# Kernel optimization log

Measured on AMD Instinct MI355X. Metric: run time of the kernel, lower is better.

## Reference

```python
import jax, jax.numpy as jnp
import numpy as np

D_MODEL = 512
H = 8


def setup_inputs() -> dict:
    key = jax.random.key(0)
    ks = jax.random.split(key, 11)
    B, L, D = 8, 1024, D_MODEL
    s = 1.0 / np.sqrt(D)
    return {
        "q": jax.random.normal(ks[0], (B, L, D), jnp.float32),
        "k": jax.random.normal(ks[1], (B, L, D), jnp.float32),
        "v": jax.random.normal(ks[2], (B, L, D), jnp.float32),
        "Wq": jax.random.normal(ks[3], (D, D), jnp.float32) * s,
        "bq": jnp.zeros((D,), jnp.float32),
        "Wk": jax.random.normal(ks[4], (D, D), jnp.float32) * s,
        "bk": jnp.zeros((D,), jnp.float32),
        "Wv": jax.random.normal(ks[5], (D, D), jnp.float32) * s,
        "bv": jnp.zeros((D,), jnp.float32),
        "Wo": jax.random.normal(ks[6], (D, D), jnp.float32) * s,
        "bo": jnp.zeros((D,), jnp.float32),
    }


def _split_heads(x, h):
    B, L, D = x.shape
    return x.reshape(B, L, h, D // h).transpose(0, 2, 1, 3)  # (B,h,L,dk)


def reference(q, k, v, Wq, bq, Wk, bk, Wv, bv, Wo, bo):
    B, L, D = q.shape
    dk = D // H
    qw = q @ Wq + bq
    kw = k @ Wk + bk
    vw = q @ Wv + bv  # faithful to source bug: dense_v applied to q, not v
    qh = _split_heads(qw, H)
    kh = _split_heads(kw, H)
    vh = _split_heads(vw, H)
    scale = jnp.asarray(1.0 / np.sqrt(dk), qh.dtype)
    scores = jnp.einsum("bhqd,bhkd->bhqk", qh, kh) * scale  # (B,h,L,L)
    attn = jax.nn.softmax(scores, axis=-1)
    ctx = jnp.einsum("bhqk,bhkd->bhqd", attn, vh)  # (B,h,L,dk)
    out = ctx.transpose(0, 2, 1, 3).reshape(B, L, D) @ Wo + bo
    return out, attn
```

## Files before the change

kernel.cpp:

```cpp
#include <hip/hip_runtime.h>

typedef unsigned short u16;
typedef __bf16 bf16x8 __attribute__((ext_vector_type(8)));
typedef unsigned short u16x8 __attribute__((ext_vector_type(8)));
typedef unsigned short u16x4 __attribute__((ext_vector_type(4)));
typedef float f32x4 __attribute__((ext_vector_type(4)));

#define MFMA16(a, b, c) __builtin_amdgcn_mfma_f32_16x16x32_bf16(a, b, c, 0, 0, 0)

__device__ __forceinline__ u16 f2bf(float f) {
    union { float f; unsigned u; } v; v.f = f;
    unsigned r = v.u + 0x7fffu + ((v.u >> 16) & 1u);
    return (u16)(r >> 16);
}

__global__ __launch_bounds__(256) void wtrans(const float* Wq, const float* Wk,
                                              const float* Wv, const float* Wo, u16* WT) {
    __shared__ float t[32][33];
    const int z = blockIdx.z;
    const float* W = (z == 0) ? Wq : (z == 1) ? Wk : (z == 2) ? Wv : Wo;
    u16* out = WT + (size_t)z * 512 * 512;
    const int tx = threadIdx.x;
    const int ty = threadIdx.y;
    const int k0 = blockIdx.y * 32;
    const int n0 = blockIdx.x * 32;
#pragma unroll
    for (int p = 0; p < 4; ++p)
        t[ty + 8 * p][tx] = W[(size_t)(k0 + ty + 8 * p) * 512 + n0 + tx];
    __syncthreads();
#pragma unroll
    for (int p = 0; p < 4; ++p) {
        const int n = n0 + ty + 8 * p;
        out[(size_t)n * 512 + k0 + tx] = f2bf(t[tx][ty + 8 * p]);
    }
}

template <bool A_F32, bool C_F32>
__device__ __forceinline__ void gemm_core(const void* Ap, const u16* Bt,
                                          const float* bias, void* Cp,
                                          int bm, int bn) {
    __shared__ u16 As[128 * 72];
    __shared__ u16 Bs[128 * 72];
    const int tid  = threadIdx.x;
    const int lane = tid & 63;
    const int w    = tid >> 6;
    const int wm   = (w >> 1) * 64;
    const int wn   = (w & 1) * 64;
    const int col  = lane & 15;
    const int quad = lane >> 4;

    f32x4 acc[4][4] = {};

    for (int kt = 0; kt < 512; kt += 64) {
        __syncthreads();
        if (A_F32) {
            const float* Af = (const float*)Ap;
            const int kg = (tid & 15) * 4;
            const int r0 = tid >> 4;
#pragma unroll
            for (int p = 0; p < 8; ++p) {
                const int r = r0 + p * 16;
                const float4 vv = *(const float4*)(Af + (size_t)(bm * 128 + r) * 512 + kt + kg);
                u16x4 o4;
                o4[0] = f2bf(vv.x); o4[1] = f2bf(vv.y); o4[2] = f2bf(vv.z); o4[3] = f2bf(vv.w);
                *(u16x4*)(As + r * 72 + kg) = o4;
            }
        } else {
            const u16* Ab = (const u16*)Ap;
            const int kg = (tid & 7) * 8;
            const int r0 = tid >> 3;
#pragma unroll
            for (int p = 0; p < 4; ++p) {
                const int r = r0 + p * 32;
                const u16x8 vv = *(const u16x8*)(Ab + (size_t)(bm * 128 + r) * 512 + kt + kg);
                *(u16x8*)(As + r * 72 + kg) = vv;
            }
        }
        {
            const int kg = (tid & 7) * 8;
            const int r0 = tid >> 3;
#pragma unroll
            for (int p = 0; p < 4; ++p) {
                const int n = r0 + p * 32;
                const u16x8 vv = *(const u16x8*)(Bt + (size_t)(bn * 128 + n) * 512 + kt + kg);
                *(u16x8*)(Bs + n * 72 + kg) = vv;
            }
        }
        __syncthreads();
#pragma unroll
        for (int ks = 0; ks < 2; ++ks) {
            const int k0 = ks * 32 + quad * 8;
            bf16x8 af[4], bfr[4];
#pragma unroll
            for (int i = 0; i < 4; ++i)
                af[i] = __builtin_bit_cast(bf16x8, *(const u16x8*)(As + (wm + i * 16 + col) * 72 + k0));
#pragma unroll
            for (int j = 0; j < 4; ++j)
                bfr[j] = __builtin_bit_cast(bf16x8, *(const u16x8*)(Bs + (wn + j * 16 + col) * 72 + k0));
#pragma unroll
            for (int i = 0; i < 4; ++i)
#pragma unroll
                for (int j = 0; j < 4; ++j)
                    acc[i][j] = MFMA16(af[i], bfr[j], acc[i][j]);
        }
    }
#pragma unroll
    for (int j = 0; j < 4; ++j) {
        const int gn = bn * 128 + wn + j * 16 + col;
        const float bv = bias[gn];
#pragma unroll
        for (int i = 0; i < 4; ++i) {
#pragma unroll
            for (int r = 0; r < 4; ++r) {
                const int gm = bm * 128 + wm + i * 16 + quad * 4 + r;
                const float val = acc[i][j][r] + bv;
                if (C_F32) ((float*)Cp)[(size_t)gm * 512 + gn] = val;
                else       ((u16*)Cp)[(size_t)gm * 512 + gn]   = f2bf(val);
            }
        }
    }
}

__global__ __launch_bounds__(256) void qkv_gemm(const float* q, const float* k, const u16* WT,
                                                const float* bq, const float* bk, const float* bv,
                                                u16* out) {
    const int z = blockIdx.z;
    const float* A    = (z == 1) ? k : q;
    const u16* B      = WT + (size_t)z * 512 * 512;
    const float* bias = (z == 0) ? bq : (z == 1) ? bk : bv;
    u16* C            = out + (size_t)z * 8192 * 512;
    gemm_core<true, false>(A, B, bias, C, blockIdx.x, blockIdx.y);
}

__global__ __launch_bounds__(256) void out_gemm(const u16* ctx, const u16* WoT,
                                                const float* bo, float* out) {
    gemm_core<false, true>(ctx, WoT, bo, out, blockIdx.x, blockIdx.y);
}

__global__ __launch_bounds__(256) void attn_kernel(const u16* qw, const u16* kw, const u16* vw,
                                                   float* attn_out, u16* ctx) {
    __shared__ u16 Qs[128 * 72];
    __shared__ u16 Ks[64 * 72];
    __shared__ u16 Vt[64 * 72];
    __shared__ u16 Ps[4][32 * 72];

    const int qt  = blockIdx.x;
    const int bh  = blockIdx.y;
    const int b   = bh >> 3, h = bh & 7;
    const int tid = threadIdx.x;
    const int lane = tid & 63, w = tid >> 6;
    const int col = lane & 15, quad = lane >> 4;
    const int wq  = w * 32;
    const float scale = 0.125f;

    const size_t headbase = (size_t)b * 1024 * 512 + (size_t)h * 64;

    {
        const int kg = (tid & 7) * 8;
        const int r0 = tid >> 3;
#pragma unroll
        for (int p = 0; p < 4; ++p) {
            const int r = r0 + p * 32;
            const u16x8 vv = *(const u16x8*)(qw + headbase + (size_t)(qt * 128 + r) * 512 + kg);
            *(u16x8*)(Qs + r * 72 + kg) = vv;
        }
    }

    float m_i[2][4], l_i[2][4];
#pragma unroll
    for (int i = 0; i < 2; ++i)
#pragma unroll
        for (int r = 0; r < 4; ++r) { m_i[i][r] = -1e30f; l_i[i][r] = 0.f; }

    for (int kt = 0; kt < 16; ++kt) {
        __syncthreads();
        {
            const int kg = (tid & 7) * 8;
            const int r0 = tid >> 3;
#pragma unroll
            for (int p = 0; p < 2; ++p) {
                const int key = r0 + p * 32;
                const u16x8 vv = *(const u16x8*)(kw + headbase + (size_t)(kt * 64 + key) * 512 + kg);
                *(u16x8*)(Ks + key * 72 + kg) = vv;
            }
        }
        __syncthreads();
        f32x4 s[2][4] = {};
#pragma unroll
        for (int ks = 0; ks < 2; ++ks) {
            const int k0 = ks * 32 + quad * 8;
            bf16x8 qf[2], kf[4];
#pragma unroll
            for (int i = 0; i < 2; ++i)
                qf[i] = __builtin_bit_cast(bf16x8, *(const u16x8*)(Qs + (wq + i * 16 + col) * 72 + k0));
#pragma unroll
            for (int j = 0; j < 4; ++j)
                kf[j] = __builtin_bit_cast(bf16x8, *(const u16x8*)(Ks + (j * 16 + col) * 72 + k0));
#pragma unroll
            for (int i = 0; i < 2; ++i)
#pragma unroll
                for (int j = 0; j < 4; ++j)
                    s[i][j] = MFMA16(qf[i], kf[j], s[i][j]);
        }
#pragma unroll
        for (int i = 0; i < 2; ++i) {
#pragma unroll
            for (int r = 0; r < 4; ++r) {
                float tm = fmaxf(fmaxf(s[i][0][r], s[i][1][r]), fmaxf(s[i][2][r], s[i][3][r])) * scale;
                tm = fmaxf(tm, __shfl_xor(tm, 1));
                tm = fmaxf(tm, __shfl_xor(tm, 2));
                tm = fmaxf(tm, __shfl_xor(tm, 4));
                tm = fmaxf(tm, __shfl_xor(tm, 8));
                const float mn = fmaxf(m_i[i][r], tm);
                float ps = 0.f;
#pragma unroll
                for (int j = 0; j < 4; ++j) ps += __expf(s[i][j][r] * scale - mn);
                ps += __shfl_xor(ps, 1);
                ps += __shfl_xor(ps, 2);
                ps += __shfl_xor(ps, 4);
                ps += __shfl_xor(ps, 8);
                const float alpha = __expf(m_i[i][r] - mn);
                l_i[i][r] = l_i[i][r] * alpha + ps;
                m_i[i][r] = mn;
            }
        }
    }

    float rinv[2][4];
#pragma unroll
    for (int i = 0; i < 2; ++i)
#pragma unroll
        for (int r = 0; r < 4; ++r) rinv[i][r] = 1.0f / l_i[i][r];

    f32x4 o[2][4] = {};

    for (int kt = 0; kt < 16; ++kt) {
        __syncthreads();
        {
            const int kg = (tid & 7) * 8;
            const int r0 = tid >> 3;
#pragma unroll
            for (int p = 0; p < 2; ++p) {
                const int key = r0 + p * 32;
                const u16x8 vv = *(const u16x8*)(kw + headbase + (size_t)(kt * 64 + key) * 512 + kg);
                *(u16x8*)(Ks + key * 72 + kg) = vv;
            }
        }
        {
            const int key = tid & 63;
            const int ob  = tid >> 6;
#pragma unroll
            for (int p = 0; p < 2; ++p) {
                const int oct = ob + 4 * p;
                const u16x8 vv = *(const u16x8*)(vw + headbase + (size_t)(kt * 64 + key) * 512 + oct * 8);
#pragma unroll
                for (int e = 0; e < 8; ++e)
                    Vt[(oct * 8 + e) * 72 + key] = vv[e];
            }
        }
        __syncthreads();
        f32x4 s[2][4] = {};
#pragma unroll
        for (int ks = 0; ks < 2; ++ks) {
            const int k0 = ks * 32 + quad * 8;
            bf16x8 qf[2], kf[4];
#pragma unroll
            for (int i = 0; i < 2; ++i)
                qf[i] = __builtin_bit_cast(bf16x8, *(const u16x8*)(Qs + (wq + i * 16 + col) * 72 + k0));
#pragma unroll
            for (int j = 0; j < 4; ++j)
                kf[j] = __builtin_bit_cast(bf16x8, *(const u16x8*)(Ks + (j * 16 + col) * 72 + k0));
#pragma unroll
            for (int i = 0; i < 2; ++i)
#pragma unroll
                for (int j = 0; j < 4; ++j)
                    s[i][j] = MFMA16(qf[i], kf[j], s[i][j]);
        }
        const size_t abase = ((size_t)bh * 1024 + (size_t)(qt * 128)) * 1024 + (size_t)kt * 64;
#pragma unroll
        for (int i = 0; i < 2; ++i) {
#pragma unroll
            for (int j = 0; j < 4; ++j) {
                const int kk = j * 16 + col;
#pragma unroll
                for (int r = 0; r < 4; ++r) {
                    const int qm = wq + i * 16 + quad * 4 + r;
                    const float p = __expf(s[i][j][r] * scale - m_i[i][r]) * rinv[i][r];
                    attn_out[abase + (size_t)qm * 1024 + kk] = p;
                    Ps[w][(i * 16 + quad * 4 + r) * 72 + kk] = f2bf(p);
                }
            }
        }
        bf16x8 vfrag[2][4];
#pragma unroll
        for (int ks = 0; ks < 2; ++ks) {
            const int k0 = ks * 32 + quad * 8;
#pragma unroll
            for (int j = 0; j < 4; ++j)
                vfrag[ks][j] = __builtin_bit_cast(bf16x8, *(const u16x8*)(Vt + (j * 16 + col) * 72 + k0));
        }
#pragma unroll
        for (int i = 0; i < 2; ++i) {
#pragma unroll
            for (int ks = 0; ks < 2; ++ks) {
                const int k0 = ks * 32 + quad * 8;
                const bf16x8 pf = __builtin_bit_cast(bf16x8, *(const u16x8*)(&Ps[w][(i * 16 + col) * 72 + k0]));
#pragma unroll
                for (int j = 0; j < 4; ++j)
                    o[i][j] = MFMA16(pf, vfrag[ks][j], o[i][j]);
            }
        }
    }

#pragma unroll
    for (int i = 0; i < 2; ++i)
#pragma unroll
        for (int j = 0; j < 4; ++j)
#pragma unroll
            for (int r = 0; r < 4; ++r) {
                const int qg = qt * 128 + wq + i * 16 + quad * 4 + r;
                const int dk = j * 16 + col;
                ctx[(size_t)(b * 1024 + qg) * 512 + h * 64 + dk] = f2bf(o[i][j][r]);
            }
}

extern "C" void kernel_launch(void* const* d_in, const int* in_sizes, int n_in,
                              void* d_out, int out_size, void* d_ws, size_t ws_size,
                              hipStream_t stream) {
    (void)in_sizes; (void)n_in; (void)out_size; (void)ws_size;
    const float* q  = (const float*)d_in[0];
    const float* k  = (const float*)d_in[1];
    const float* Wq = (const float*)d_in[3];
    const float* bq = (const float*)d_in[4];
    const float* Wk = (const float*)d_in[5];
    const float* bk = (const float*)d_in[6];
    const float* Wv = (const float*)d_in[7];
    const float* bv = (const float*)d_in[8];
    const float* Wo = (const float*)d_in[9];
    const float* bo = (const float*)d_in[10];

    float* out  = (float*)d_out;
    float* attn = (float*)d_out + (size_t)8 * 1024 * 512;

    char* ws = (char*)d_ws;
    u16* WT  = (u16*)ws;
    u16* qkv = (u16*)(ws + (size_t)4 * 512 * 512 * 2);
    u16* qw  = qkv;
    u16* kw  = qkv + (size_t)8192 * 512;
    u16* vw  = qkv + (size_t)2 * 8192 * 512;
    u16* ctx = (u16*)(ws + (size_t)4 * 512 * 512 * 2 + (size_t)3 * 8192 * 512 * 2);

    wtrans   <<<dim3(16, 16, 4), dim3(32, 8), 0, stream>>>(Wq, Wk, Wv, Wo, WT);
    qkv_gemm <<<dim3(64, 4, 3),  256,          0, stream>>>(q, k, WT, bq, bk, bv, qkv);
    attn_kernel<<<dim3(8, 64),   256,          0, stream>>>(qw, kw, vw, attn, ctx);
    out_gemm <<<dim3(64, 4),     256,          0, stream>>>(ctx, WT + (size_t)3 * 512 * 512, bo, out);
}
```

Measured before the change: 451.5 us.

## Restructure attention to 8 waves, drop max tracking, vectorize attn stores, preconvert inputs

The attention kernel moves to 512 threads, with each wave owning 16 query rows and keeping its Q fragments in registers instead of shared memory. The first pass no longer tracks a running max and only sums unshifted exponentials. Probabilities are staged through shared memory so the attention matrix can be written with float4 stores. A separate kernel converts q and k to bf16 once, so the GEMM loads bf16 directly, and the GEMMs get occupancy hints. Skipping the max subtraction risks overflow for large scores, and the written attention values are now bf16-rounded.

```diff
diff --git a/kernel.cpp b/kernel.cpp
--- a/kernel.cpp
+++ b/kernel.cpp
@@ -12,6 +12,10 @@
     union { float f; unsigned u; } v; v.f = f;
     unsigned r = v.u + 0x7fffu + ((v.u >> 16) & 1u);
     return (u16)(r >> 16);
+}
+__device__ __forceinline__ float bf2f(u16 u) {
+    union { unsigned u; float f; } v; v.u = (unsigned)u << 16;
+    return v.f;
 }
 
 __global__ __launch_bounds__(256) void wtrans(const float* Wq, const float* Wk,
@@ -20,10 +24,8 @@
     const int z = blockIdx.z;
     const float* W = (z == 0) ? Wq : (z == 1) ? Wk : (z == 2) ? Wv : Wo;
     u16* out = WT + (size_t)z * 512 * 512;
-    const int tx = threadIdx.x;
-    const int ty = threadIdx.y;
-    const int k0 = blockIdx.y * 32;
-    const int n0 = blockIdx.x * 32;
+    const int tx = threadIdx.x, ty = threadIdx.y;
+    const int k0 = blockIdx.y * 32, n0 = blockIdx.x * 32;
 #pragma unroll
     for (int p = 0; p < 4; ++p)
         t[ty + 8 * p][tx] = W[(size_t)(k0 + ty + 8 * p) * 512 + n0 + tx];
@@ -35,8 +37,19 @@
     }
 }
 
-template <bool A_F32, bool C_F32>
-__device__ __forceinline__ void gemm_core(const void* Ap, const u16* Bt,
+__global__ __launch_bounds__(256) void qkconv(const float* q, const float* k, u16* qb, u16* kb) {
+    const size_t n4 = (size_t)8192 * 512 / 4;
+    const size_t stride = (size_t)gridDim.x * 256;
+    for (size_t i = (size_t)blockIdx.x * 256 + threadIdx.x; i < 2 * n4; i += stride) {
+        const float4 v = (i < n4) ? ((const float4*)q)[i] : ((const float4*)k)[i - n4];
+        u16x4 o;
+        o[0] = f2bf(v.x); o[1] = f2bf(v.y); o[2] = f2bf(v.z); o[3] = f2bf(v.w);
+        if (i < n4) ((u16x4*)qb)[i] = o; else ((u16x4*)kb)[i - n4] = o;
+    }
+}
+
+template <bool C_F32>
+__device__ __forceinline__ void gemm_core(const u16* A, const u16* Bt,
                                           const float* bias, void* Cp,
                                           int bm, int bn) {
     __shared__ u16 As[128 * 72];
@@ -53,37 +66,16 @@
 
     for (int kt = 0; kt < 512; kt += 64) {
         __syncthreads();
-        if (A_F32) {
-            const float* Af = (const float*)Ap;
-            const int kg = (tid & 15) * 4;
-            const int r0 = tid >> 4;
-#pragma unroll
-            for (int p = 0; p < 8; ++p) {
-                const int r = r0 + p * 16;
-                const float4 vv = *(const float4*)(Af + (size_t)(bm * 128 + r) * 512 + kt + kg);
-                u16x4 o4;
-                o4[0] = f2bf(vv.x); o4[1] = f2bf(vv.y); o4[2] = f2bf(vv.z); o4[3] = f2bf(vv.w);
-                *(u16x4*)(As + r * 72 + kg) = o4;
-            }
-        } else {
-            const u16* Ab = (const u16*)Ap;
+        {
             const int kg = (tid & 7) * 8;
             const int r0 = tid >> 3;
 #pragma unroll
             for (int p = 0; p < 4; ++p) {
                 const int r = r0 + p * 32;
-                const u16x8 vv = *(const u16x8*)(Ab + (size_t)(bm * 128 + r) * 512 + kt + kg);
-                *(u16x8*)(As + r * 72 + kg) = vv;
-            }
-        }
-        {
-            const int kg = (tid & 7) * 8;
-            const int r0 = tid >> 3;
-#pragma unroll
-            for (int p = 0; p < 4; ++p) {
-                const int n = r0 + p * 32;
-                const u16x8 vv = *(const u16x8*)(Bt + (size_t)(bn * 128 + n) * 512 + kt + kg);
-                *(u16x8*)(Bs + n * 72 + kg) = vv;
+                *(u16x8*)(As + r * 72 + kg) =
+                    *(const u16x8*)(A + (size_t)(bm * 128 + r) * 512 + kt + kg);
+                *(u16x8*)(Bs + r * 72 + kg) =
+                    *(const u16x8*)(Bt + (size_t)(bn * 128 + r) * 512 + kt + kg);
             }
         }
         __syncthreads();
@@ -121,28 +113,27 @@
     }
 }
 
-__global__ __launch_bounds__(256) void qkv_gemm(const float* q, const float* k, const u16* WT,
-                                                const float* bq, const float* bk, const float* bv,
-                                                u16* out) {
+__global__ __launch_bounds__(256, 3) void qkv_gemm(const u16* qb, const u16* kb, const u16* WT,
+                                                   const float* bq, const float* bk, const float* bv,
+                                                   u16* out) {
     const int z = blockIdx.z;
-    const float* A    = (z == 1) ? k : q;
+    const u16* A      = (z == 1) ? kb : qb;
     const u16* B      = WT + (size_t)z * 512 * 512;
     const float* bias = (z == 0) ? bq : (z == 1) ? bk : bv;
     u16* C            = out + (size_t)z * 8192 * 512;
-    gemm_core<true, false>(A, B, bias, C, blockIdx.x, blockIdx.y);
-}
-
-__global__ __launch_bounds__(256) void out_gemm(const u16* ctx, const u16* WoT,
-                                                const float* bo, float* out) {
-    gemm_core<false, true>(ctx, WoT, bo, out, blockIdx.x, blockIdx.y);
-}
-
-__global__ __launch_bounds__(256) void attn_kernel(const u16* qw, const u16* kw, const u16* vw,
-                                                   float* attn_out, u16* ctx) {
-    __shared__ u16 Qs[128 * 72];
+    gemm_core<false>(A, B, bias, C, blockIdx.x, blockIdx.y);
+}
+
+__global__ __launch_bounds__(256, 3) void out_gemm(const u16* ctx, const u16* WoT,
+                                                   const float* bo, float* out) {
+    gemm_core<true>(ctx, WoT, bo, out, blockIdx.x, blockIdx.y);
+}
+
+__global__ __launch_bounds__(512, 4) void attn_kernel(const u16* qw, const u16* kw, const u16* vw,
+                                                      float* attn_out, u16* ctx) {
     __shared__ u16 Ks[64 * 72];
     __shared__ u16 Vt[64 * 72];
-    __shared__ u16 Ps[4][32 * 72];
+    __shared__ u16 Ps[8][16 * 72];
 
     const int qt  = blockIdx.x;
     const int bh  = blockIdx.y;
@@ -150,178 +141,120 @@
     const int tid = threadIdx.x;
     const int lane = tid & 63, w = tid >> 6;
     const int col = lane & 15, quad = lane >> 4;
-    const int wq  = w * 32;
+    const int wq  = w * 16;
     const float scale = 0.125f;
 
     const size_t headbase = (size_t)b * 1024 * 512 + (size_t)h * 64;
 
+    bf16x8 qf[2];
     {
-        const int kg = (tid & 7) * 8;
-        const int r0 = tid >> 3;
-#pragma unroll
-        for (int p = 0; p < 4; ++p) {
-            const int r = r0 + p * 32;
-            const u16x8 vv = *(const u16x8*)(qw + headbase + (size_t)(qt * 128 + r) * 512 + kg);
-            *(u16x8*)(Qs + r * 72 + kg) = vv;
-        }
-    }
-
-    float m_i[2][4], l_i[2][4];
-#pragma unroll
-    for (int i = 0; i < 2; ++i)
-#pragma unroll
-        for (int r = 0; r < 4; ++r) { m_i[i][r] = -1e30f; l_i[i][r] = 0.f; }
+        const size_t qrow = headbase + (size_t)(qt * 128 + wq + col) * 512 + quad * 8;
+        qf[0] = __builtin_bit_cast(bf16x8, *(const u16x8*)(qw + qrow));
+        qf[1] = __builtin_bit_cast(bf16x8, *(const u16x8*)(qw + qrow + 32));
+    }
+
+    float l_acc[4] = {0.f, 0.f, 0.f, 0.f};
 
     for (int kt = 0; kt < 16; ++kt) {
         __syncthreads();
         {
-            const int kg = (tid & 7) * 8;
-            const int r0 = tid >> 3;
-#pragma unroll
-            for (int p = 0; p < 2; ++p) {
-                const int key = r0 + p * 32;
-                const u16x8 vv = *(const u16x8*)(kw + headbase + (size_t)(kt * 64 + key) * 512 + kg);
-                *(u16x8*)(Ks + key * 72 + kg) = vv;
-            }
-        }
-        __syncthreads();
-        f32x4 s[2][4] = {};
-#pragma unroll
-        for (int ks = 0; ks < 2; ++ks) {
-            const int k0 = ks * 32 + quad * 8;
-            bf16x8 qf[2], kf[4];
-#pragma unroll
-            for (int i = 0; i < 2; ++i)
-                qf[i] = __builtin_bit_cast(bf16x8, *(const u16x8*)(Qs + (wq + i * 16 + col) * 72 + k0));
+            const int key = tid >> 3, kg = (tid & 7) * 8;
+            *(u16x8*)(Ks + key * 72 + kg) =
+                *(const u16x8*)(kw + headbase + (size_t)(kt * 64 + key) * 512 + kg);
+        }
+        __syncthreads();
+        f32x4 s[4] = {};
+#pragma unroll
+        for (int ks = 0; ks < 2; ++ks) {
+            const int k0 = ks * 32 + quad * 8;
+            bf16x8 kf[4];
 #pragma unroll
             for (int j = 0; j < 4; ++j)
                 kf[j] = __builtin_bit_cast(bf16x8, *(const u16x8*)(Ks + (j * 16 + col) * 72 + k0));
 #pragma unroll
-            for (int i = 0; i < 2; ++i)
-#pragma unroll
-                for (int j = 0; j < 4; ++j)
-                    s[i][j] = MFMA16(qf[i], kf[j], s[i][j]);
-        }
-#pragma unroll
-        for (int i = 0; i < 2; ++i) {
+            for (int j = 0; j < 4; ++j)
+                s[j] = MFMA16(qf[ks], kf[j], s[j]);
+        }
+#pragma unroll
+        for (int r = 0; r < 4; ++r)
+            l_acc[r] += __expf(s[0][r] * scale) + __expf(s[1][r] * scale) +
+                        __expf(s[2][r] * scale) + __expf(s[3][r] * scale);
+    }
+
+    float rinv[4];
+#pragma unroll
+    for (int r = 0; r < 4; ++r) {
+        float l = l_acc[r];
+        l += __shfl_xor(l, 1); l += __shfl_xor(l, 2);
+        l += __shfl_xor(l, 4); l += __shfl_xor(l, 8);
+        rinv[r] = 1.0f / l;
+    }
+
+    f32x4 o[4] = {};
+
+    for (int kt = 0; kt < 16; ++kt) {
+        __syncthreads();
+        {
+            const int key = tid >> 3, kg = (tid & 7) * 8;
+            *(u16x8*)(Ks + key * 72 + kg) =
+                *(const u16x8*)(kw + headbase + (size_t)(kt * 64 + key) * 512 + kg);
+        }
+        {
+            const int key = tid & 63, oct = tid >> 6;
+            const u16x8 vv = *(const u16x8*)(vw + headbase + (size_t)(kt * 64 + key) * 512 + oct * 8);
+#pragma unroll
+            for (int e = 0; e < 8; ++e)
+                Vt[(oct * 8 + e) * 72 + key] = vv[e];
+        }
+        __syncthreads();
+        f32x4 s[4] = {};
+#pragma unroll
+        for (int ks = 0; ks < 2; ++ks) {
+            const int k0 = ks * 32 + quad * 8;
+            bf16x8 kf[4];
+#pragma unroll
+            for (int j = 0; j < 4; ++j)
+                kf[j] = __builtin_bit_cast(bf16x8, *(const u16x8*)(Ks + (j * 16 + col) * 72 + k0));
+#pragma unroll
+            for (int j = 0; j < 4; ++j)
+                s[j] = MFMA16(qf[ks], kf[j], s[j]);
+        }
+#pragma unroll
+        for (int j = 0; j < 4; ++j)
 #pragma unroll
             for (int r = 0; r < 4; ++r) {
-                float tm = fmaxf(fmaxf(s[i][0][r], s[i][1][r]), fmaxf(s[i][2][r], s[i][3][r])) * scale;
-                tm = fmaxf(tm, __shfl_xor(tm, 1));
-                tm = fmaxf(tm, __shfl_xor(tm, 2));
-                tm = fmaxf(tm, __shfl_xor(tm, 4));
-                tm = fmaxf(tm, __shfl_xor(tm, 8));
-                const float mn = fmaxf(m_i[i][r], tm);
-                float ps = 0.f;
-#pragma unroll
-                for (int j = 0; j < 4; ++j) ps += __expf(s[i][j][r] * scale - mn);
-                ps += __shfl_xor(ps, 1);
-                ps += __shfl_xor(ps, 2);
-                ps += __shfl_xor(ps, 4);
-                ps += __shfl_xor(ps, 8);
-                const float alpha = __expf(m_i[i][r] - mn);
-                l_i[i][r] = l_i[i][r] * alpha + ps;
-                m_i[i][r] = mn;
-            }
-        }
-    }
-
-    float rinv[2][4];
-#pragma unroll
-    for (int i = 0; i < 2; ++i)
-#pragma unroll
-        for (int r = 0; r < 4; ++r) rinv[i][r] = 1.0f / l_i[i][r];
-
-    f32x4 o[2][4] = {};
-
-    for (int kt = 0; kt < 16; ++kt) {
-        __syncthreads();
-        {
-            const int kg = (tid & 7) * 8;
-            const int r0 = tid >> 3;
-#pragma unroll
-            for (int p = 0; p < 2; ++p) {
-                const int key = r0 + p * 32;
-                const u16x8 vv = *(const u16x8*)(kw + headbase + (size_t)(kt * 64 + key) * 512 + kg);
-                *(u16x8*)(Ks + key * 72 + kg) = vv;
-            }
-        }
-        {
-            const int key = tid & 63;
-            const int ob  = tid >> 6;
-#pragma unroll
-            for (int p = 0; p < 2; ++p) {
-                const int oct = ob + 4 * p;
-                const u16x8 vv = *(const u16x8*)(vw + headbase + (size_t)(kt * 64 + key) * 512 + oct * 8);
-#pragma unroll
-                for (int e = 0; e < 8; ++e)
-                    Vt[(oct * 8 + e) * 72 + key] = vv[e];
-            }
-        }
-        __syncthreads();
-        f32x4 s[2][4] = {};
-#pragma unroll
-        for (int ks = 0; ks < 2; ++ks) {
-            const int k0 = ks * 32 + quad * 8;
-            bf16x8 qf[2], kf[4];
-#pragma unroll
-            for (int i = 0; i < 2; ++i)
-                qf[i] = __builtin_bit_cast(bf16x8, *(const u16x8*)(Qs + (wq + i * 16 + col) * 72 + k0));
-#pragma unroll
-            for (int j = 0; j < 4; ++j)
-                kf[j] = __builtin_bit_cast(bf16x8, *(const u16x8*)(Ks + (j * 16 + col) * 72 + k0));
-#pragma unroll
-            for (int i = 0; i < 2; ++i)
-#pragma unroll
-                for (int j = 0; j < 4; ++j)
-                    s[i][j] = MFMA16(qf[i], kf[j], s[i][j]);
-        }
-        const size_t abase = ((size_t)bh * 1024 + (size_t)(qt * 128)) * 1024 + (size_t)kt * 64;
-#pragma unroll
-        for (int i = 0; i < 2; ++i) {
+                const float p = __expf(s[j][r] * scale) * rinv[r];
+                Ps[w][(quad * 4 + r) * 72 + j * 16 + col] = f2bf(p);
+            }
+        const int c4 = col * 4;
+#pragma unroll
+        for (int it = 0; it < 4; ++it) {
+            const int rl = it * 4 + quad;
+            const u16x4 pv = *(const u16x4*)(&Ps[w][rl * 72 + c4]);
+            float4 f;
+            f.x = bf2f(pv[0]); f.y = bf2f(pv[1]); f.z = bf2f(pv[2]); f.w = bf2f(pv[3]);
+            *(float4*)(attn_out + ((size_t)bh * 1024 + qt * 128 + wq + rl) * 1024
+                       + (size_t)kt * 64 + c4) = f;
+        }
+#pragma unroll
+        for (int ks = 0; ks < 2; ++ks) {
+            const int k0 = ks * 32 + quad * 8;
+            const bf16x8 pf = __builtin_bit_cast(bf16x8, *(const u16x8*)(&Ps[w][col * 72 + k0]));
 #pragma unroll
             for (int j = 0; j < 4; ++j) {
-                const int kk = j * 16 + col;
-#pragma unroll
-                for (int r = 0; r < 4; ++r) {
-                    const int qm = wq + i * 16 + quad * 4 + r;
-                    const float p = __expf(s[i][j][r] * scale - m_i[i][r]) * rinv[i][r];
-                    attn_out[abase + (size_t)qm * 1024 + kk] = p;
-                    Ps[w][(i * 16 + quad * 4 + r) * 72 + kk] = f2bf(p);
-                }
-            }
-        }
-        bf16x8 vfrag[2][4];
-#pragma unroll
-        for (int ks = 0; ks < 2; ++ks) {
-            const int k0 = ks * 32 + quad * 8;
-#pragma unroll
-            for (int j = 0; j < 4; ++j)
-                vfrag[ks][j] = __builtin_bit_cast(bf16x8, *(const u16x8*)(Vt + (j * 16 + col) * 72 + k0));
-        }
-#pragma unroll
-        for (int i = 0; i < 2; ++i) {
-#pragma unroll
-            for (int ks = 0; ks < 2; ++ks) {
-                const int k0 = ks * 32 + quad * 8;
-                const bf16x8 pf = __builtin_bit_cast(bf16x8, *(const u16x8*)(&Ps[w][(i * 16 + col) * 72 + k0]));
-#pragma unroll
-                for (int j = 0; j < 4; ++j)
-                    o[i][j] = MFMA16(pf, vfrag[ks][j], o[i][j]);
-            }
-        }
-    }
-
-#pragma unroll
-    for (int i = 0; i < 2; ++i)
-#pragma unroll
-        for (int j = 0; j < 4; ++j)
-#pragma unroll
-            for (int r = 0; r < 4; ++r) {
-                const int qg = qt * 128 + wq + i * 16 + quad * 4 + r;
-                const int dk = j * 16 + col;
-                ctx[(size_t)(b * 1024 + qg) * 512 + h * 64 + dk] = f2bf(o[i][j][r]);
-            }
+                const bf16x8 vf = __builtin_bit_cast(bf16x8, *(const u16x8*)(Vt + (j * 16 + col) * 72 + k0));
+                o[j] = MFMA16(pf, vf, o[j]);
+            }
+        }
+    }
+
+#pragma unroll
+    for (int j = 0; j < 4; ++j)
+#pragma unroll
+        for (int r = 0; r < 4; ++r) {
+            const int qg = qt * 128 + wq + quad * 4 + r;
+            ctx[(size_t)(b * 1024 + qg) * 512 + h * 64 + j * 16 + col] = f2bf(o[j][r]);
+        }
 }
 
 extern "C" void kernel_launch(void* const* d_in, const int* in_sizes, int n_in,
@@ -344,14 +277,17 @@
 
     char* ws = (char*)d_ws;
     u16* WT  = (u16*)ws;
-    u16* qkv = (u16*)(ws + (size_t)4 * 512 * 512 * 2);
+    u16* qb  = (u16*)(ws + (size_t)2 * 1024 * 1024);
+    u16* kb  = qb + (size_t)8192 * 512;
+    u16* qkv = kb + (size_t)8192 * 512;
     u16* qw  = qkv;
     u16* kw  = qkv + (size_t)8192 * 512;
     u16* vw  = qkv + (size_t)2 * 8192 * 512;
-    u16* ctx = (u16*)(ws + (size_t)4 * 512 * 512 * 2 + (size_t)3 * 8192 * 512 * 2);
-
-    wtrans   <<<dim3(16, 16, 4), dim3(32, 8), 0, stream>>>(Wq, Wk, Wv, Wo, WT);
-    qkv_gemm <<<dim3(64, 4, 3),  256,          0, stream>>>(q, k, WT, bq, bk, bv, qkv);
-    attn_kernel<<<dim3(8, 64),   256,          0, stream>>>(qw, kw, vw, attn, ctx);
-    out_gemm <<<dim3(64, 4),     256,          0, stream>>>(ctx, WT + (size_t)3 * 512 * 512, bo, out);
-}
+    u16* ctx = qkv + (size_t)3 * 8192 * 512;
+
+    wtrans     <<<dim3(16, 16, 4), dim3(32, 8), 0, stream>>>(Wq, Wk, Wv, Wo, WT);
+    qkconv     <<<dim3(2048),      256,          0, stream>>>(q, k, qb, kb);
+    qkv_gemm   <<<dim3(64, 4, 3),  256,          0, stream>>>(qb, kb, WT, bq, bk, bv, qkv);
+    attn_kernel<<<dim3(8, 64),     512,          0, stream>>>(qw, kw, vw, attn, ctx);
+    out_gemm   <<<dim3(64, 4),     256,          0, stream>>>(ctx, WT + (size_t)3 * 512 * 512, bo, out);
+}
```

After: 441.4 us. 2.2% less time.
